# Optimization experiments

Measured on AMD Instinct MI355X. Metric: run time of the kernel, lower is better.

Reference implementation:

```python
import jax, jax.numpy as jnp
import numpy as np

DIM = 1024
NUM_HEADS = 16
HEAD_DIM = DIM // NUM_HEADS
SCALE = HEAD_DIM ** -0.5


def setup_inputs() -> dict:
    key = jax.random.key(0)
    k1, k2, k3, k4, k5 = jax.random.split(key, 5)
    B, N, C = 2, 2048, DIM
    x = jax.random.normal(k1, (B, N, C), dtype=jnp.float32)
    # nn.Linear(dim, 3*dim, bias=False): weight shape [3*dim, dim]
    w_qkv = jax.random.normal(k2, (3 * C, C), dtype=jnp.float32) * (C ** -0.5)
    # nn.Linear(dim, dim): weight [dim, dim], bias [dim]
    w_proj = jax.random.normal(k3, (C, C), dtype=jnp.float32) * (C ** -0.5)
    b_proj = jax.random.normal(k4, (C,), dtype=jnp.float32) * 0.02
    return {"x": x, "w_qkv": w_qkv, "w_proj": w_proj, "b_proj": b_proj}


def reference(x, w_qkv, w_proj, b_proj):
    B, N, C = x.shape
    H, D = NUM_HEADS, HEAD_DIM
    # qkv: [B, N, 3C] -> [3, B, H, N, D]
    qkv = (x @ w_qkv.T).reshape(B, N, 3, H, D).transpose(2, 0, 3, 1, 4)
    q, k, v = qkv[0], qkv[1], qkv[2]
    # attention scores [B, H, N, N]
    attn = jnp.einsum("bhnd,bhmd->bhnm", q, k) * SCALE
    attn = jax.nn.softmax(attn, axis=-1)
    # dropout p=0.0 -> identity (eval mode)
    out = jnp.einsum("bhnm,bhmd->bhnd", attn, v)  # [B, H, N, D]
    out = out.transpose(0, 2, 1, 3).reshape(B, N, C)
    return out @ w_proj.T + b_proj
```

## Files before the change

kernel.cpp:

```cpp
#include <hip/hip_runtime.h>
#include <hip/hip_bf16.h>
#include <cstdint>

#define DEV __device__ __forceinline__

typedef float f32x4 __attribute__((ext_vector_type(4)));
typedef short bf16x8 __attribute__((ext_vector_type(8)));
typedef unsigned short u16;
typedef unsigned int u32;

constexpr int Bb = 2, Nn = 2048, Cc = 1024, Hh = 16, Dd = 64;
constexpr float QSCALE = 0.18033688011112042f;

DEV u16 f2b(float f) {
  unsigned u = __float_as_uint(f);
  u += 0x7FFFu + ((u >> 16) & 1u);
  return (u16)(u >> 16);
}

DEV void gload_lds16(const u16* g, u16* l) {
  __builtin_amdgcn_global_load_lds(
      (const __attribute__((address_space(1))) void*)g,
      (__attribute__((address_space(3))) void*)l, 16, 0, 0);
}

DEV int swz(int row, int byteInRow) {
  return row * 128 + (byteInRow ^ ((row & 7) << 4));
}

DEV u32 cvtpk(float lo, float hi) {
  u32 r;
  asm("v_cvt_pk_bf16_f32 %0, %1, %2" : "=v"(r) : "v"(lo), "v"(hi));
  return r;
}
DEV void pl32swap(u32& a, u32& b) {
  asm("v_permlane32_swap_b32 %0, %1" : "+v"(a), "+v"(b));
}
DEV void pl16swap(u32& a, u32& b) {
  asm("v_permlane16_swap_b32 %0, %1" : "+v"(a), "+v"(b));
}

#if __has_builtin(__builtin_amdgcn_exp2f)
DEV float fast_exp2(float x) { return __builtin_amdgcn_exp2f(x); }
#else
DEV float fast_exp2(float x) { return exp2f(x); }
#endif

__global__ void cvt_all(const float* __restrict__ x, u16* __restrict__ xb,
                        const float* __restrict__ wq, u16* __restrict__ wqb,
                        const float* __restrict__ wp, u16* __restrict__ wpb) {
  constexpr int n1 = 4096 * 1024 / 4, n2 = 3072 * 1024 / 4, n3 = 1024 * 1024 / 4;
  int idx = blockIdx.x * blockDim.x + threadIdx.x;
  int stride = gridDim.x * blockDim.x;
  for (int i = idx; i < n1 + n2 + n3; i += stride) {
    const float* in; u16* out; int j;
    if (i < n1) { in = x; out = xb; j = i; }
    else if (i < n1 + n2) { in = wq; out = wqb; j = i - n1; }
    else { in = wp; out = wpb; j = i - n1 - n2; }
    float4 v = ((const float4*)in)[j];
    ushort4 o;
    o.x = f2b(v.x); o.y = f2b(v.y); o.z = f2b(v.z); o.w = f2b(v.w);
    ((ushort4*)out)[j] = o;
  }
}

template <int MODE>
__global__ __launch_bounds__(256) void gemm_bt(
    const u16* __restrict__ A, const u16* __restrict__ W, int K, int Nmat,
    u16* __restrict__ qkv_out, float* __restrict__ fout, const float* __restrict__ bias) {
  __shared__ __align__(16) u16 As[128 * 32];
  __shared__ __align__(16) u16 Bs[128 * 32];
  const int t = threadIdx.x;
  const int lane = t & 63;
  const int wm = t >> 7, wn = (t >> 6) & 1;
  const int m0 = blockIdx.y * 128, n0 = blockIdx.x * 128;

  const int sr = t >> 2;
  const int sc = (t & 3) * 8;
  const u16* gA = A + (size_t)(m0 + sr) * K + sc;
  const u16* gW = W + (size_t)(n0 + sr) * K + sc;
  u16* lA = As + t * 8;
  u16* lB = Bs + t * 8;

  const int fr = lane & 15;
  const int fk = (lane >> 4) * 8;

  f32x4 acc[4][4] = {};

  for (int k0 = 0; k0 < K; k0 += 32) {
    gload_lds16(gA + k0, lA);
    gload_lds16(gA + k0 + (size_t)64 * K, lA + 2048);
    gload_lds16(gW + k0, lB);
    gload_lds16(gW + k0 + (size_t)64 * K, lB + 2048);
    __syncthreads();
    bf16x8 af[4], bf[4];
#pragma unroll
    for (int i = 0; i < 4; ++i)
      af[i] = *(const bf16x8*)&As[(wm * 64 + i * 16 + fr) * 32 + fk];
#pragma unroll
    for (int j = 0; j < 4; ++j)
      bf[j] = *(const bf16x8*)&Bs[(wn * 64 + j * 16 + fr) * 32 + fk];
#pragma unroll
    for (int i = 0; i < 4; ++i)
#pragma unroll
      for (int j = 0; j < 4; ++j)
        acc[i][j] = __builtin_amdgcn_mfma_f32_16x16x32_bf16(af[i], bf[j], acc[i][j], 0, 0, 0);
    __syncthreads();
  }

  const int rg = (lane >> 4) * 4;
#pragma unroll
  for (int i = 0; i < 4; ++i) {
#pragma unroll
    for (int j = 0; j < 4; ++j) {
      const int col = n0 + wn * 64 + j * 16 + fr;
#pragma unroll
      for (int r = 0; r < 4; ++r) {
        const int row = m0 + wm * 64 + i * 16 + rg + r;
        float v = acc[i][j][r];
        if (MODE == 0) {
          const int s = col >> 10, h = (col >> 6) & 15, d = col & 63;
          const int b = row >> 11, n = row & 2047;
          size_t off;
          if (s == 2) {
            off = (size_t)2 * Bb * Hh * Nn * Dd + (((size_t)b * Hh + h) * Dd + d) * Nn + n;
          } else {
            if (s == 0) v *= QSCALE;
            off = ((((size_t)s * Bb + b) * Hh + h) * Nn + n) * Dd + d;
          }
          qkv_out[off] = f2b(v);
        } else {
          fout[(size_t)row * Nmat + col] = v + bias[col];
        }
      }
    }
  }
}

__global__ __launch_bounds__(256, 2) void attn_fwd(
    const u16* __restrict__ Qg, const u16* __restrict__ Kg,
    const u16* __restrict__ Vtg, u16* __restrict__ Og) {
  __shared__ __align__(16) char smem[34816];
  const int t = threadIdx.x, lane = t & 63, w = t >> 6;
  const int qg = w >> 1, kh = w & 1;
  const int wg = ((blockIdx.x & 7) << 6) | (blockIdx.x >> 3);
  const int bh = wg >> 4;
  const int q0 = (wg & 15) * 128;
  const size_t base = (size_t)bh * Nn * Dd;
  const u16* Qb = Qg + base;
  const u16* Kb = Kg + base;
  const u16* Vb = Vtg + base;
  const int fr = lane & 15, g = lane >> 4;

  bf16x8 onesv;
  {
    union { u32 u[4]; bf16x8 v; } o_;
#pragma unroll
    for (int i = 0; i < 4; ++i) o_.u[i] = 0x3F803F80u;
    onesv = o_.v;
  }

  bf16x8 qf[4][2];
#pragma unroll
  for (int qt = 0; qt < 4; ++qt)
#pragma unroll
    for (int dc = 0; dc < 2; ++dc)
      qf[qt][dc] = *(const bf16x8*)&Qb[(size_t)(q0 + qg * 64 + qt * 16 + fr) * 64 + dc * 32 + g * 8];

  f32x4 ot[4][4] = {};
  float lse[4] = {0.f, 0.f, 0.f, 0.f};

  const int srow = t >> 3, scb = t & 7;
  const u16* kp = Kb + srow * 64 + scb * 8;
  const u16* vp = Vb + (size_t)srow * Nn + scb * 8;
  uint4 kreg[2], vreg[2];

#define LOADT(tile)                                                   \
  {                                                                   \
    kreg[0] = *(const uint4*)(kp + (size_t)(tile) * 4096);            \
    kreg[1] = *(const uint4*)(kp + (size_t)(tile) * 4096 + 2048);     \
    vreg[0] = *(const uint4*)(vp + (size_t)(tile) * 64);              \
    vreg[1] = *(const uint4*)(vp + (size_t)(tile) * 64 + 32 * Nn);    \
  }
#define STORET(buf)                                                   \
  {                                                                   \
    char* kb_ = smem + (buf) * 16384;                                 \
    char* vb_ = kb_ + 8192;                                           \
    *(uint4*)(kb_ + swz(srow, scb * 16)) = kreg[0];                   \
    *(uint4*)(kb_ + swz(srow + 32, scb * 16)) = kreg[1];              \
    *(uint4*)(vb_ + swz(srow, scb * 16)) = vreg[0];                   \
    *(uint4*)(vb_ + swz(srow + 32, scb * 16)) = vreg[1];              \
  }

  LOADT(0);
  STORET(0);
  __syncthreads();

  for (int it = 0; it < 32; ++it) {
    const int cur = it & 1;
    const char* Kst = smem + cur * 16384;
    const char* Vst = Kst + 8192;
    if (it < 31) LOADT(it + 1);

    bf16x8 kf[2][2];
#pragma unroll
    for (int kvt = 0; kvt < 2; ++kvt)
#pragma unroll
      for (int dc = 0; dc < 2; ++dc)
        kf[kvt][dc] = *(const bf16x8*)(Kst + swz(kh * 32 + kvt * 16 + fr, dc * 64 + g * 16));
    f32x4 st[2][4] = {};
    __builtin_amdgcn_s_setprio(1);
#pragma unroll
    for (int dc = 0; dc < 2; ++dc)
#pragma unroll
      for (int kvt = 0; kvt < 2; ++kvt)
#pragma unroll
        for (int qt = 0; qt < 4; ++qt)
          st[kvt][qt] = __builtin_amdgcn_mfma_f32_16x16x32_bf16(kf[kvt][dc], qf[qt][dc], st[kvt][qt], 0, 0, 0);
    __builtin_amdgcn_s_setprio(0);

#pragma unroll
    for (int kvt = 0; kvt < 2; ++kvt)
#pragma unroll
      for (int qt = 0; qt < 4; ++qt)
#pragma unroll
        for (int r = 0; r < 4; ++r)
          st[kvt][qt][r] = fast_exp2(st[kvt][qt][r]);

    u32 pw[4][4];
#pragma unroll
    for (int qt = 0; qt < 4; ++qt) {
      u32 a0 = cvtpk(st[0][qt][0], st[0][qt][1]);
      u32 a1 = cvtpk(st[0][qt][2], st[0][qt][3]);
      u32 b0 = cvtpk(st[1][qt][0], st[1][qt][1]);
      u32 b1 = cvtpk(st[1][qt][2], st[1][qt][3]);
      pl32swap(a0, b0); pl16swap(a0, b0);
      pl32swap(a1, b1); pl16swap(a1, b1);
      pw[qt][0] = a0; pw[qt][1] = a1; pw[qt][2] = b0; pw[qt][3] = b1;
    }

    bf16x8 vf[4];
#pragma unroll
    for (int dt = 0; dt < 4; ++dt)
      vf[dt] = *(const bf16x8*)(Vst + swz(dt * 16 + fr, kh * 64 + g * 16));
    __builtin_amdgcn_s_setprio(1);
#pragma unroll
    for (int qt = 0; qt < 4; ++qt) {
      union { u32 u[4]; bf16x8 v; } pu;
      pu.u[0] = pw[qt][0]; pu.u[1] = pw[qt][1]; pu.u[2] = pw[qt][2]; pu.u[3] = pw[qt][3];
      f32x4 z = {0.f, 0.f, 0.f, 0.f};
      f32x4 rsv = __builtin_amdgcn_mfma_f32_16x16x32_bf16(onesv, pu.v, z, 0, 0, 0);
      lse[qt] += rsv[0];
#pragma unroll
      for (int dt = 0; dt < 4; ++dt)
        ot[dt][qt] = __builtin_amdgcn_mfma_f32_16x16x32_bf16(vf[dt], pu.v, ot[dt][qt], 0, 0, 0);
    }
    __builtin_amdgcn_s_setprio(0);

    if (it < 31) {
      STORET(cur ^ 1);
      __syncthreads();
    }
  }

  __syncthreads();
  float* Ob = (float*)(smem + qg * 16896);
  float* Lb = (float*)(smem + 33792 + qg * 256);
  if (kh) {
#pragma unroll
    for (int qt = 0; qt < 4; ++qt) {
#pragma unroll
      for (int dt = 0; dt < 4; ++dt)
#pragma unroll
        for (int r = 0; r < 4; ++r)
          Ob[(qt * 16 + fr) * 66 + dt * 16 + 4 * g + r] = ot[dt][qt][r];
      if (g == 0) Lb[qt * 16 + fr] = lse[qt];
    }
  }
  __syncthreads();
  if (!kh) {
    const int b = bh >> 4, h = bh & 15;
#pragma unroll
    for (int qt = 0; qt < 4; ++qt) {
      const float inv = 1.f / (lse[qt] + Lb[qt * 16 + fr]);
      const int tok = q0 + qg * 64 + qt * 16 + fr;
      const size_t rowbase = ((size_t)b * Nn + tok) * Cc + h * 64;
#pragma unroll
      for (int dt = 0; dt < 4; ++dt) {
        ushort4 o4;
        o4.x = f2b((ot[dt][qt][0] + Ob[(qt * 16 + fr) * 66 + dt * 16 + 4 * g + 0]) * inv);
        o4.y = f2b((ot[dt][qt][1] + Ob[(qt * 16 + fr) * 66 + dt * 16 + 4 * g + 1]) * inv);
        o4.z = f2b((ot[dt][qt][2] + Ob[(qt * 16 + fr) * 66 + dt * 16 + 4 * g + 2]) * inv);
        o4.w = f2b((ot[dt][qt][3] + Ob[(qt * 16 + fr) * 66 + dt * 16 + 4 * g + 3]) * inv);
        *(ushort4*)&Og[rowbase + dt * 16 + g * 4] = o4;
      }
    }
  }
#undef LOADT
#undef STORET
}

extern "C" void kernel_launch(void* const* d_in, const int* in_sizes, int n_in,
                              void* d_out, int out_size, void* d_ws, size_t ws_size,
                              hipStream_t stream) {
  const float* x      = (const float*)d_in[0];
  const float* w_qkv  = (const float*)d_in[1];
  const float* w_proj = (const float*)d_in[2];
  const float* b_proj = (const float*)d_in[3];
  float* out = (float*)d_out;

  u16* xb     = (u16*)d_ws;
  u16* wqkvb  = xb + (size_t)4096 * 1024;
  u16* wprojb = wqkvb + (size_t)3072 * 1024;
  u16* qkv    = wprojb + (size_t)1024 * 1024;
  u16* ows    = qkv + (size_t)3 * Bb * Hh * Nn * Dd;
  u16* q  = qkv;
  u16* k  = qkv + (size_t)Bb * Hh * Nn * Dd;
  u16* vt = k + (size_t)Bb * Hh * Nn * Dd;

  cvt_all<<<2048, 256, 0, stream>>>(x, xb, w_qkv, wqkvb, w_proj, wprojb);
  gemm_bt<0><<<dim3(24, 32), 256, 0, stream>>>(xb, wqkvb, 1024, 3072, qkv, nullptr, nullptr);
  attn_fwd<<<512, 256, 0, stream>>>(q, k, vt, ows);
  gemm_bt<1><<<dim3(8, 32), 256, 0, stream>>>(ows, wprojb, 1024, 1024, nullptr, out, b_proj);
}
```

Before: 126.2 us.

## Rewrite QKV and projection GEMMs with larger tiles, double buffering, swizzled LDS

The QKV GEMM now uses 256x256 tiles with 512 threads, BK=64, double-buffered LDS staging, an XOR-swizzled layout and a grouped block order for L2 locality. The projection GEMM keeps 128x128 tiles but adds double buffering, a new swizzle for its 64-byte rows and block remapping. Both raise MFMA priority with s_setprio. These target global-load latency, LDS bank conflicts and per-iteration barrier stalls. The cost is much more shared memory and register pressure, plus a QKV grid of only 192 blocks, which may underfill the GPU's compute units.

```diff
diff --git a/kernel.cpp b/kernel.cpp
--- a/kernel.cpp
+++ b/kernel.cpp
@@ -26,6 +26,9 @@
 
 DEV int swz(int row, int byteInRow) {
   return row * 128 + (byteInRow ^ ((row & 7) << 4));
+}
+DEV int swzp(int row, int byteInRow) {
+  return row * 64 + (byteInRow ^ ((((row >> 2) + row) & 3) << 4));
 }
 
 DEV u32 cvtpk(float lo, float hi) {
@@ -64,77 +67,158 @@
   }
 }
 
-template <int MODE>
-__global__ __launch_bounds__(256) void gemm_bt(
-    const u16* __restrict__ A, const u16* __restrict__ W, int K, int Nmat,
-    u16* __restrict__ qkv_out, float* __restrict__ fout, const float* __restrict__ bias) {
-  __shared__ __align__(16) u16 As[128 * 32];
-  __shared__ __align__(16) u16 Bs[128 * 32];
-  const int t = threadIdx.x;
-  const int lane = t & 63;
+__global__ __launch_bounds__(512, 2) void gemm256_qkv(
+    const u16* __restrict__ A, const u16* __restrict__ W, u16* __restrict__ qkv_out) {
+  constexpr int K = 1024, NT = K / 64;
+  __shared__ __align__(16) u16 Ab[2][256 * 64];
+  __shared__ __align__(16) u16 Bbuf[2][256 * 64];
+  const int t = threadIdx.x, lane = t & 63;
+  const int w = t >> 6, wm = w >> 2, wn = w & 3;
+  const int bid = blockIdx.x;
+  const int wg = (bid & 7) * 24 + (bid >> 3);
+  const int bx = wg % 12, by = wg / 12;
+  const int m0 = by * 256, n0 = bx * 256;
+  const int fr = lane & 15, g = lane >> 4;
+
+  const int srow = t >> 3;
+  const int scp = (t & 7) ^ (srow & 7);
+  const u16* gA = A + (size_t)(m0 + srow) * K + scp * 8;
+  const u16* gW = W + (size_t)(n0 + srow) * K + scp * 8;
+
+  f32x4 acc[8][4] = {};
+
+#define STAGE256(tile, buf)                                                     \
+  {                                                                             \
+    const int k0_ = (tile) * 64;                                                \
+    _Pragma("unroll")                                                           \
+    for (int i = 0; i < 4; ++i)                                                 \
+      gload_lds16(gA + k0_ + (size_t)i * 64 * K, &Ab[buf][t * 8 + i * 4096]);   \
+    _Pragma("unroll")                                                           \
+    for (int i = 0; i < 4; ++i)                                                 \
+      gload_lds16(gW + k0_ + (size_t)i * 64 * K, &Bbuf[buf][t * 8 + i * 4096]); \
+  }
+
+  STAGE256(0, 0);
+  __syncthreads();
+
+  for (int tt = 0; tt < NT; ++tt) {
+    const int cur = tt & 1;
+    if (tt + 1 < NT) STAGE256(tt + 1, cur ^ 1);
+    const char* Ac = (const char*)Ab[cur];
+    const char* Bc = (const char*)Bbuf[cur];
+#pragma unroll
+    for (int kh = 0; kh < 2; ++kh) {
+      bf16x8 af[8], bfr[4];
+#pragma unroll
+      for (int mi = 0; mi < 8; ++mi)
+        af[mi] = *(const bf16x8*)(Ac + swz(wm * 128 + mi * 16 + fr, kh * 64 + g * 16));
+#pragma unroll
+      for (int ni = 0; ni < 4; ++ni)
+        bfr[ni] = *(const bf16x8*)(Bc + swz(wn * 64 + ni * 16 + fr, kh * 64 + g * 16));
+      __builtin_amdgcn_s_setprio(1);
+#pragma unroll
+      for (int mi = 0; mi < 8; ++mi)
+#pragma unroll
+        for (int ni = 0; ni < 4; ++ni)
+          acc[mi][ni] = __builtin_amdgcn_mfma_f32_16x16x32_bf16(af[mi], bfr[ni], acc[mi][ni], 0, 0, 0);
+      __builtin_amdgcn_s_setprio(0);
+    }
+    __syncthreads();
+  }
+
+#pragma unroll
+  for (int mi = 0; mi < 8; ++mi) {
+#pragma unroll
+    for (int ni = 0; ni < 4; ++ni) {
+      const int col = n0 + wn * 64 + ni * 16 + fr;
+      const int s = col >> 10, h = (col >> 6) & 15, d = col & 63;
+#pragma unroll
+      for (int r = 0; r < 4; ++r) {
+        const int row = m0 + wm * 128 + mi * 16 + g * 4 + r;
+        const int b = row >> 11, n = row & 2047;
+        float v = acc[mi][ni][r];
+        size_t off;
+        if (s == 2) {
+          off = (size_t)2 * Bb * Hh * Nn * Dd + (((size_t)b * Hh + h) * Dd + d) * Nn + n;
+        } else {
+          if (s == 0) v *= QSCALE;
+          off = ((((size_t)s * Bb + b) * Hh + h) * Nn + n) * Dd + d;
+        }
+        qkv_out[off] = f2b(v);
+      }
+    }
+  }
+#undef STAGE256
+}
+
+__global__ __launch_bounds__(256) void gemm_proj(
+    const u16* __restrict__ A, const u16* __restrict__ W,
+    float* __restrict__ fout, const float* __restrict__ bias) {
+  constexpr int K = 1024, Nmat = 1024, NT = K / 32;
+  __shared__ __align__(16) u16 As[2][128 * 32];
+  __shared__ __align__(16) u16 Bs[2][128 * 32];
+  const int t = threadIdx.x, lane = t & 63;
   const int wm = t >> 7, wn = (t >> 6) & 1;
-  const int m0 = blockIdx.y * 128, n0 = blockIdx.x * 128;
-
-  const int sr = t >> 2;
-  const int sc = (t & 3) * 8;
-  const u16* gA = A + (size_t)(m0 + sr) * K + sc;
-  const u16* gW = W + (size_t)(n0 + sr) * K + sc;
-  u16* lA = As + t * 8;
-  u16* lB = Bs + t * 8;
-
-  const int fr = lane & 15;
-  const int fk = (lane >> 4) * 8;
+  const int bid = blockIdx.x;
+  const int wg = (bid & 7) * 32 + (bid >> 3);
+  const int bx = wg & 7, by = wg >> 3;
+  const int m0 = by * 128, n0 = bx * 128;
+  const int fr = lane & 15, g = lane >> 4;
+
+  const int srow = t >> 2;
+  const int scp = (t & 3) ^ (((t >> 2) + (t >> 4)) & 3);
+  const u16* gA = A + (size_t)(m0 + srow) * K + scp * 8;
+  const u16* gW = W + (size_t)(n0 + srow) * K + scp * 8;
 
   f32x4 acc[4][4] = {};
 
-  for (int k0 = 0; k0 < K; k0 += 32) {
-    gload_lds16(gA + k0, lA);
-    gload_lds16(gA + k0 + (size_t)64 * K, lA + 2048);
-    gload_lds16(gW + k0, lB);
-    gload_lds16(gW + k0 + (size_t)64 * K, lB + 2048);
+#define STAGEP(tile, buf)                                              \
+  {                                                                    \
+    const int k0_ = (tile) * 32;                                       \
+    gload_lds16(gA + k0_, &As[buf][t * 8]);                            \
+    gload_lds16(gA + k0_ + (size_t)64 * K, &As[buf][t * 8 + 2048]);    \
+    gload_lds16(gW + k0_, &Bs[buf][t * 8]);                            \
+    gload_lds16(gW + k0_ + (size_t)64 * K, &Bs[buf][t * 8 + 2048]);    \
+  }
+
+  STAGEP(0, 0);
+  __syncthreads();
+
+  for (int tt = 0; tt < NT; ++tt) {
+    const int cur = tt & 1;
+    if (tt + 1 < NT) STAGEP(tt + 1, cur ^ 1);
+    const char* Ac = (const char*)As[cur];
+    const char* Bc = (const char*)Bs[cur];
+    bf16x8 af[4], bfr[4];
+#pragma unroll
+    for (int i = 0; i < 4; ++i)
+      af[i] = *(const bf16x8*)(Ac + swzp(wm * 64 + i * 16 + fr, g * 16));
+#pragma unroll
+    for (int j = 0; j < 4; ++j)
+      bfr[j] = *(const bf16x8*)(Bc + swzp(wn * 64 + j * 16 + fr, g * 16));
+    __builtin_amdgcn_s_setprio(1);
+#pragma unroll
+    for (int i = 0; i < 4; ++i)
+#pragma unroll
+      for (int j = 0; j < 4; ++j)
+        acc[i][j] = __builtin_amdgcn_mfma_f32_16x16x32_bf16(af[i], bfr[j], acc[i][j], 0, 0, 0);
+    __builtin_amdgcn_s_setprio(0);
     __syncthreads();
-    bf16x8 af[4], bf[4];
-#pragma unroll
-    for (int i = 0; i < 4; ++i)
-      af[i] = *(const bf16x8*)&As[(wm * 64 + i * 16 + fr) * 32 + fk];
-#pragma unroll
-    for (int j = 0; j < 4; ++j)
-      bf[j] = *(const bf16x8*)&Bs[(wn * 64 + j * 16 + fr) * 32 + fk];
-#pragma unroll
-    for (int i = 0; i < 4; ++i)
-#pragma unroll
-      for (int j = 0; j < 4; ++j)
-        acc[i][j] = __builtin_amdgcn_mfma_f32_16x16x32_bf16(af[i], bf[j], acc[i][j], 0, 0, 0);
-    __syncthreads();
-  }
-
-  const int rg = (lane >> 4) * 4;
-#pragma unroll
-  for (int i = 0; i < 4; ++i) {
+  }
+
+  const int rg = g * 4;
+#pragma unroll
+  for (int i = 0; i < 4; ++i)
 #pragma unroll
     for (int j = 0; j < 4; ++j) {
       const int col = n0 + wn * 64 + j * 16 + fr;
 #pragma unroll
       for (int r = 0; r < 4; ++r) {
         const int row = m0 + wm * 64 + i * 16 + rg + r;
-        float v = acc[i][j][r];
-        if (MODE == 0) {
-          const int s = col >> 10, h = (col >> 6) & 15, d = col & 63;
-          const int b = row >> 11, n = row & 2047;
-          size_t off;
-          if (s == 2) {
-            off = (size_t)2 * Bb * Hh * Nn * Dd + (((size_t)b * Hh + h) * Dd + d) * Nn + n;
-          } else {
-            if (s == 0) v *= QSCALE;
-            off = ((((size_t)s * Bb + b) * Hh + h) * Nn + n) * Dd + d;
-          }
-          qkv_out[off] = f2b(v);
-        } else {
-          fout[(size_t)row * Nmat + col] = v + bias[col];
-        }
+        fout[(size_t)row * Nmat + col] = acc[i][j][r] + bias[col];
       }
     }
-  }
+#undef STAGEP
 }
 
 __global__ __launch_bounds__(256, 2) void attn_fwd(
@@ -319,7 +403,7 @@
   u16* vt = k + (size_t)Bb * Hh * Nn * Dd;
 
   cvt_all<<<2048, 256, 0, stream>>>(x, xb, w_qkv, wqkvb, w_proj, wprojb);
-  gemm_bt<0><<<dim3(24, 32), 256, 0, stream>>>(xb, wqkvb, 1024, 3072, qkv, nullptr, nullptr);
+  gemm256_qkv<<<192, 512, 0, stream>>>(xb, wqkvb, qkv);
   attn_fwd<<<512, 256, 0, stream>>>(q, k, vt, ows);
-  gemm_bt<1><<<dim3(8, 32), 256, 0, stream>>>(ows, wprojb, 1024, 1024, nullptr, out, b_proj);
-}
+  gemm_proj<<<256, 256, 0, stream>>>(ows, wprojb, out, b_proj);
+}
```

Result: slower. 141.4 us (+12.0%).
